# Optimization experiments

Measured on AMD Instinct MI355X. Metric: run time of the kernel, lower is better.

The kernel has to match this reference:

```python
import jax, jax.numpy as jnp
import numpy as np

B, S, HID, H, D = 4, 1024, 1024, 16, 64
MAXP = 1024  # max_position_embeddings
EPS = 1e-8


def setup_inputs() -> dict:
    key = jax.random.key(0)
    ks = jax.random.split(key, 9)
    scale = 0.02  # keep logits small since masked_softmax has no max-subtraction
    return {
        "hidden_states": jax.random.normal(ks[0], (B, S, HID), jnp.float32),
        "attention_mask": jnp.zeros((B, 1, 1, S), jnp.float32),
        "skim_mask": jax.random.randint(ks[1], (B, S), 0, 2, jnp.int32),
        "Wq": jax.random.normal(ks[2], (HID, HID), jnp.float32) * scale,
        "bq": jnp.zeros((HID,), jnp.float32),
        "Wk": jax.random.normal(ks[3], (HID, HID), jnp.float32) * scale,
        "bk": jnp.zeros((HID,), jnp.float32),
        "Wv": jax.random.normal(ks[4], (HID, HID), jnp.float32) * scale,
        "bv": jnp.zeros((HID,), jnp.float32),
        "dist_emb": jax.random.normal(ks[5], (2 * MAXP - 1, D), jnp.float32) * scale,
    }


def reference(hidden_states, attention_mask, skim_mask, Wq, bq, Wk, bk, Wv, bv, dist_emb):
    # Linear projections (W stored as [in, out]) then split heads: [B,H,S,D]
    def heads(x):
        return x.reshape(B, S, H, D).transpose(0, 2, 1, 3)

    q = heads(hidden_states @ Wq + bq)
    k = heads(hidden_states @ Wk + bk)
    v = heads(hidden_states @ Wv + bv)

    # raw scores [B,H,S,S]
    scores = jnp.einsum('bhld,bhrd->bhlr', q, k)

    # relative_key positional bias
    pos = jnp.arange(S)
    distance = pos[:, None] - pos[None, :]                 # [S,S]
    pe = dist_emb[distance + MAXP - 1]                     # [S,S,D]
    scores = scores + jnp.einsum('bhld,lrd->bhlr', q, pe)

    scores = scores / jnp.sqrt(jnp.float32(D))
    scores = scores + attention_mask

    # skim_mask branch: masked_softmax (exp * mask, normalized with eps)
    mask = skim_mask[:, None, None, :].astype(scores.dtype)  # [B,1,1,S]
    exps = jnp.exp(scores) * mask
    probs = exps / (EPS + exps.sum(-1, keepdims=True))
    # dropout in eval mode -> identity

    ctx = jnp.einsum('bhlr,bhrd->bhld', probs, v)
    return ctx.transpose(0, 2, 1, 3).reshape(B, S, HID)
```

## Files before the change

### kernel.cpp

```cpp
#include <hip/hip_runtime.h>
#include <hip/hip_bf16.h>


#define EPSV 1e-8f

typedef short bfrag __attribute__((ext_vector_type(8)));
typedef float cfrag __attribute__((ext_vector_type(16)));
typedef int v2i __attribute__((ext_vector_type(2)));
typedef float v2f __attribute__((ext_vector_type(2)));

__device__ __forceinline__ short f2bf(float f) {
    __hip_bfloat16 h = __float2bfloat16(f);
    return *reinterpret_cast<short*>(&h);
}
__device__ __forceinline__ unsigned int pk2(short a, short b) {
    return (unsigned int)(unsigned short)a | ((unsigned int)(unsigned short)b << 16);
}

__global__ __launch_bounds__(256) void prep(
    const float* __restrict__ hidden, const float* __restrict__ Wq,
    const float* __restrict__ Wk, const float* __restrict__ Wv,
    const float* __restrict__ dist,
    short* __restrict__ Xs, short* __restrict__ Wt, short* __restrict__ Db)
{
    __shared__ short Tl[32 * 72];
    const int bid = blockIdx.x, tid = threadIdx.x;

    if (bid < 2048) {
        const int mt = bid >> 4, kg = bid & 15;
        const int m_l = tid >> 3, k8 = (tid & 7) * 8;
        const float* src = hidden + (size_t)(mt * 32 + m_l) * 1024 + kg * 64 + k8;
        float4 v0 = *(const float4*)src, v1 = *(const float4*)(src + 4);
        short o[8];
        o[0] = f2bf(v0.x); o[1] = f2bf(v0.y); o[2] = f2bf(v0.z); o[3] = f2bf(v0.w);
        o[4] = f2bf(v1.x); o[5] = f2bf(v1.y); o[6] = f2bf(v1.z); o[7] = f2bf(v1.w);
        *(bfrag*)&Tl[m_l * 72 + k8] = *(bfrag*)o;
        __syncthreads();
        const int l31 = tid & 31, q2 = (tid >> 5) & 1, kc = tid >> 6;
        bfrag r = *(const bfrag*)&Tl[l31 * 72 + kc * 16 + q2 * 8];
        *(bfrag*)(Xs + ((size_t)(mt * 64 + kg * 4 + kc) * 64 + q2 * 32 + l31) * 8) = r;
    } else if (bid < 3584) {
        const int t = bid - 2048, z = t >> 9, nt = (t >> 4) & 31, kg = t & 15;
        const float* W = (z == 0) ? Wq : ((z == 1) ? Wk : Wv);
        const int k_l = tid >> 2, n8 = (tid & 3) * 8;
        const float* src = W + (size_t)(kg * 64 + k_l) * 1024 + nt * 32 + n8;
        float4 v0 = *(const float4*)src, v1 = *(const float4*)(src + 4);
        float vv[8] = {v0.x, v0.y, v0.z, v0.w, v1.x, v1.y, v1.z, v1.w};
#pragma unroll
        for (int i = 0; i < 8; i++)
            Tl[(n8 + i) * 72 + k_l] = f2bf(vv[i]);
        __syncthreads();
        const int l31 = tid & 31, q2 = (tid >> 5) & 1, kc = tid >> 6;
        bfrag r = *(const bfrag*)&Tl[l31 * 72 + kc * 16 + q2 * 8];
        *(bfrag*)(Wt + (size_t)z * 1048576
                  + ((size_t)(nt * 64 + kg * 4 + kc) * 64 + q2 * 32 + l31) * 8) = r;
    } else {
        const int idx = (bid - 3584) * 256 + tid;
        if (idx < 16376) {
            const float* src = dist + (size_t)idx * 8;
            float4 v0 = *(const float4*)src, v1 = *(const float4*)(src + 4);
            short o[8];
            o[0] = f2bf(v0.x); o[1] = f2bf(v0.y); o[2] = f2bf(v0.z); o[3] = f2bf(v0.w);
            o[4] = f2bf(v1.x); o[5] = f2bf(v1.y); o[6] = f2bf(v1.z); o[7] = f2bf(v1.w);
            *(bfrag*)(Db + (size_t)idx * 8) = *(bfrag*)o;
        }
    }
}

__global__ __launch_bounds__(256) void qkv_mfma(
    const short* __restrict__ Xs, const short* __restrict__ Wt,
    const float* __restrict__ bq, const float* __restrict__ bk,
    const float* __restrict__ bv,
    short* __restrict__ Qf, short* __restrict__ Kf, short* __restrict__ Vt)
{
    const int z = blockIdx.z;
    const short* W = Wt + (size_t)z * 1048576;
    const float* bias = (z == 0) ? bq : ((z == 1) ? bk : bv);
    const float scale = (z == 0) ? 0.18033688011112042f : 1.0f;

    const int tid = threadIdx.x, lane = tid & 63, wid = tid >> 6;
    const int q2 = lane >> 5, l31 = lane & 31;
    const int wr = wid >> 1, wc = wid & 1;
    const int m0 = blockIdx.x * 128, n0 = blockIdx.y * 128;

    cfrag acc[2][2];
#pragma unroll
    for (int i = 0; i < 2; i++)
#pragma unroll
        for (int j = 0; j < 2; j++)
#pragma unroll
            for (int e = 0; e < 16; e++) acc[i][j][e] = 0.f;

    const short* ap0 = Xs + ((size_t)((m0 >> 5) + wr * 2 + 0) * 64 * 64 + lane) * 8;
    const short* ap1 = Xs + ((size_t)((m0 >> 5) + wr * 2 + 1) * 64 * 64 + lane) * 8;
    const short* bp0 = W  + ((size_t)((n0 >> 5) + wc * 2 + 0) * 64 * 64 + lane) * 8;
    const short* bp1 = W  + ((size_t)((n0 >> 5) + wc * 2 + 1) * 64 * 64 + lane) * 8;

    bfrag a0c, a1c, b0c, b1c, a0n, a1n, b0n, b1n;
    a0c = *(const bfrag*)(ap0); a1c = *(const bfrag*)(ap1);
    b0c = *(const bfrag*)(bp0); b1c = *(const bfrag*)(bp1);

#pragma unroll 2
    for (int kc = 0; kc < 64; kc += 2) {
        {
            const int off = (kc + 1) * 512;
            a0n = *(const bfrag*)(ap0 + off); a1n = *(const bfrag*)(ap1 + off);
            b0n = *(const bfrag*)(bp0 + off); b1n = *(const bfrag*)(bp1 + off);
        }
        acc[0][0] = __builtin_amdgcn_mfma_f32_32x32x16_bf16(a0c, b0c, acc[0][0], 0, 0, 0);
        acc[0][1] = __builtin_amdgcn_mfma_f32_32x32x16_bf16(a0c, b1c, acc[0][1], 0, 0, 0);
        acc[1][0] = __builtin_amdgcn_mfma_f32_32x32x16_bf16(a1c, b0c, acc[1][0], 0, 0, 0);
        acc[1][1] = __builtin_amdgcn_mfma_f32_32x32x16_bf16(a1c, b1c, acc[1][1], 0, 0, 0);
        if (kc + 2 < 64) {
            const int off = (kc + 2) * 512;
            a0c = *(const bfrag*)(ap0 + off); a1c = *(const bfrag*)(ap1 + off);
            b0c = *(const bfrag*)(bp0 + off); b1c = *(const bfrag*)(bp1 + off);
        }
        acc[0][0] = __builtin_amdgcn_mfma_f32_32x32x16_bf16(a0n, b0n, acc[0][0], 0, 0, 0);
        acc[0][1] = __builtin_amdgcn_mfma_f32_32x32x16_bf16(a0n, b1n, acc[0][1], 0, 0, 0);
        acc[1][0] = __builtin_amdgcn_mfma_f32_32x32x16_bf16(a1n, b0n, acc[1][0], 0, 0, 0);
        acc[1][1] = __builtin_amdgcn_mfma_f32_32x32x16_bf16(a1n, b1n, acc[1][1], 0, 0, 0);
    }

#pragma unroll
    for (int nt = 0; nt < 2; nt++) {
        const int c = n0 + wc * 64 + nt * 32 + l31;
        const float bval = bias[c];
        const int h = c >> 6;
        const int d = nt * 32 + l31;
#pragma unroll
        for (int mt = 0; mt < 2; mt++) {
            const int tok0 = m0 + wr * 64 + mt * 32;
            const int bb = tok0 >> 10, s_base = tok0 & 1023;
            const size_t bhbase = (size_t)(bb * 16 + h) * 65536;
            if (z < 2) {
                short* outp = (z == 0) ? Qf : Kf;
                const size_t fbase = bhbase
                    + ((size_t)((s_base >> 5) * 4 + (d >> 4)) * 64
                       + ((d >> 3) & 1) * 32) * 8 + (d & 7);
#pragma unroll
                for (int reg = 0; reg < 16; reg++) {
                    const int row = (reg & 3) + 8 * (reg >> 2) + 4 * q2;
                    outp[fbase + (size_t)row * 8] = f2bf((acc[mt][nt][reg] + bval) * scale);
                }
            } else {
#pragma unroll
                for (int g = 0; g < 4; g++) {
                    const float e0 = acc[mt][nt][4 * g + 0] + bval;
                    const float e1 = acc[mt][nt][4 * g + 1] + bval;
                    const float e2 = acc[mt][nt][4 * g + 2] + bval;
                    const float e3 = acc[mt][nt][4 * g + 3] + bval;
                    uint2 w2;
                    w2.x = pk2(f2bf(e0), f2bf(e1));
                    w2.y = pk2(f2bf(e2), f2bf(e3));
                    const size_t flat = bhbase
                        + ((size_t)(nt * 64 + (s_base >> 4) + (g >> 1)) * 64
                           + (g & 1) * 32 + l31) * 8 + 4 * q2;
                    *(uint2*)(Vt + flat) = w2;
                }
            }
        }
    }
}

__global__ __launch_bounds__(256, 2) void attn_mfma(
    const short* __restrict__ Qf, const short* __restrict__ Kf,
    const short* __restrict__ Vt, const short* __restrict__ Db,
    const float* __restrict__ amask, const int* __restrict__ skim,
    float* __restrict__ out)
{
    __shared__ short Tb[128 * 132];
    __shared__ float Lg[1024];

    const int tid = threadIdx.x, lane = tid & 63, w = tid >> 6;
    const int q2 = lane >> 5, l31 = lane & 31;
    const int bh = blockIdx.x, b = bh >> 4, hh = bh & 15;
    const int l0 = blockIdx.y * 128;

    {
        const int r4 = tid * 4;
        float4 am = *(const float4*)(amask + b * 1024 + r4);
        int4 sk = *(const int4*)(skim + b * 1024 + r4);
        Lg[r4 + 0] = __expf(am.x) * (float)sk.x;
        Lg[r4 + 1] = __expf(am.y) * (float)sk.y;
        Lg[r4 + 2] = __expf(am.z) * (float)sk.z;
        Lg[r4 + 3] = __expf(am.w) * (float)sk.w;
    }
    __syncthreads();

    const short* Qg = Qf + (size_t)bh * 65536;
    const short* Kg = Kf + (size_t)bh * 65536;
    const short* Vg = Vt + (size_t)bh * 65536;

    bfrag qa[4];
#pragma unroll
    for (int c = 0; c < 4; c++)
        qa[c] = *(const bfrag*)(Qg + ((size_t)(((l0 >> 5) + w) * 4 + c) * 64 + lane) * 8);

    cfrag oacc[2];
#pragma unroll
    for (int mt = 0; mt < 2; mt++)
#pragma unroll
        for (int e = 0; e < 16; e++) oacc[mt][e] = 0.f;
    v2f es01 = {0.f, 0.f}, es23 = {0.f, 0.f};

    const int Lband = l0 + 32 * w;
    const int lg = Lband + l31;
    const int rowb = (32 * w + l31) * 132;

    for (int r0 = -128; r0 < 1024; r0 += 64) {
        const bool produce = r0 < 960;

        bfrag pb[2][4];
        if (produce) {
#pragma unroll
            for (int mt = 0; mt < 2; mt++) {
                const int D0 = Lband - r0 - 128 + 32 * mt;
                const int er = min(max(D0 + l31 + 1023, 0), 2046);
#pragma unroll
                for (int kc = 0; kc < 4; kc++)
                    pb[mt][kc] = *(const bfrag*)(Db + (size_t)er * 64 + kc * 16 + q2 * 8);
            }
        }

        if (r0 >= 0) {
            bfrag kb[2][4], vbl[4][2];
            v2i trr[2][4];
#pragma unroll
            for (int mt = 0; mt < 2; mt++)
#pragma unroll
                for (int kc = 0; kc < 4; kc++)
                    kb[mt][kc] = *(const bfrag*)(Kg
                        + ((size_t)(((r0 >> 5) + mt) * 4 + kc) * 64 + lane) * 8);
#pragma unroll
            for (int kc = 0; kc < 4; kc++)
#pragma unroll
                for (int mtd = 0; mtd < 2; mtd++)
                    vbl[kc][mtd] = *(const bfrag*)(Vg
                        + ((size_t)(mtd * 64 + (r0 >> 4) + kc) * 64 + lane) * 8);
#pragma unroll
            for (int mt = 0; mt < 2; mt++)
#pragma unroll
                for (int g = 0; g < 4; g++)
                    trr[mt][g] = *(const v2i*)&Tb[rowb
                        + ((r0 + 32 * mt + 8 * g + 4 * q2) & 127)];

#pragma unroll
            for (int mt = 0; mt < 2; mt++) {
                cfrag sfr;
#pragma unroll
                for (int g = 0; g < 4; g++) {
                    const v2i t2 = trr[mt][g];
                    sfr[4 * g + 0] = __builtin_bit_cast(float, (unsigned)t2[0] << 16);
                    sfr[4 * g + 1] = __builtin_bit_cast(float, (unsigned)t2[0] & 0xffff0000u);
                    sfr[4 * g + 2] = __builtin_bit_cast(float, (unsigned)t2[1] << 16);
                    sfr[4 * g + 3] = __builtin_bit_cast(float, (unsigned)t2[1] & 0xffff0000u);
                }
                __builtin_amdgcn_s_setprio(1);
#pragma unroll
                for (int kc = 0; kc < 4; kc++)
                    sfr = __builtin_amdgcn_mfma_f32_32x32x16_bf16(
                        kb[mt][kc], qa[kc], sfr, 0, 0, 0);
                __builtin_amdgcn_s_setprio(0);

                unsigned int P[4][2];
#pragma unroll
                for (int g = 0; g < 4; g++) {
                    const int rb = r0 + 32 * mt + 8 * g + 4 * q2;
                    float4 g4 = *(const float4*)&Lg[rb];
                    float ev0 = __builtin_amdgcn_exp2f(sfr[4 * g + 0]) * g4.x;
                    float ev1 = __builtin_amdgcn_exp2f(sfr[4 * g + 1]) * g4.y;
                    float ev2 = __builtin_amdgcn_exp2f(sfr[4 * g + 2]) * g4.z;
                    float ev3 = __builtin_amdgcn_exp2f(sfr[4 * g + 3]) * g4.w;
                    es01 += (v2f){ev0, ev1};
                    es23 += (v2f){ev2, ev3};
                    P[g][0] = pk2(f2bf(ev0), f2bf(ev1));
                    P[g][1] = pk2(f2bf(ev2), f2bf(ev3));
                }
#pragma unroll
                for (int c = 0; c < 2; c++) {
                    v2i s0 = __builtin_amdgcn_permlane32_swap(
                        (int)P[2 * c][0], (int)P[2 * c + 1][0], false, false);
                    v2i s1 = __builtin_amdgcn_permlane32_swap(
                        (int)P[2 * c][1], (int)P[2 * c + 1][1], false, false);
                    union { bfrag f; int d[4]; } u;
                    u.d[0] = s0[0]; u.d[1] = s1[0]; u.d[2] = s0[1]; u.d[3] = s1[1];
                    const int kc = 2 * mt + c;
                    __builtin_amdgcn_s_setprio(1);
#pragma unroll
                    for (int mtd = 0; mtd < 2; mtd++)
                        oacc[mtd] = __builtin_amdgcn_mfma_f32_32x32x16_bf16(
                            vbl[kc][mtd], u.f, oacc[mtd], 0, 0, 0);
                    __builtin_amdgcn_s_setprio(0);
                }
            }
        }

        if (produce) {
#pragma unroll
            for (int mt = 0; mt < 2; mt++) {
                cfrag t;
#pragma unroll
                for (int e = 0; e < 16; e++) t[e] = 0.f;
                __builtin_amdgcn_s_setprio(1);
#pragma unroll
                for (int kc = 0; kc < 4; kc++)
                    t = __builtin_amdgcn_mfma_f32_32x32x16_bf16(
                        pb[mt][kc], qa[kc], t, 0, 0, 0);
                __builtin_amdgcn_s_setprio(0);
#pragma unroll
                for (int e = 0; e < 16; e++) {
                    const int rr = (e & 3) + 8 * (e >> 2) + 4 * q2;
                    Tb[rowb + ((l31 + r0 - 32 * mt - rr) & 127)] = f2bf(t[e]);
                }
            }
        }
    }

    float esum = (es01[0] + es01[1]) + (es23[0] + es23[1]);
    const float den = EPSV + esum + __shfl_xor(esum, 32);
    const float inv = 1.0f / den;
    float* ob = out + ((size_t)(b * 1024 + lg) * 1024) + hh * 64;
#pragma unroll
    for (int mtd = 0; mtd < 2; mtd++) {
#pragma unroll
        for (int g = 0; g < 4; g++) {
            float4 o;
            o.x = oacc[mtd][4 * g + 0] * inv;
            o.y = oacc[mtd][4 * g + 1] * inv;
            o.z = oacc[mtd][4 * g + 2] * inv;
            o.w = oacc[mtd][4 * g + 3] * inv;
            *(float4*)(ob + 32 * mtd + 8 * g + 4 * q2) = o;
        }
    }
}

extern "C" void kernel_launch(void* const* d_in, const int* in_sizes, int n_in,
                              void* d_out, int out_size, void* d_ws, size_t ws_size,
                              hipStream_t stream) {
    const float* hidden = (const float*)d_in[0];
    const float* amask  = (const float*)d_in[1];
    const int*   skim   = (const int*)d_in[2];
    const float* Wq     = (const float*)d_in[3];
    const float* bq     = (const float*)d_in[4];
    const float* Wk     = (const float*)d_in[5];
    const float* bk     = (const float*)d_in[6];
    const float* Wv     = (const float*)d_in[7];
    const float* bv     = (const float*)d_in[8];
    const float* dist   = (const float*)d_in[9];
    float* out = (float*)d_out;

    char* w = (char*)d_ws;
    short* Xs  = (short*)(w);
    short* Wt  = (short*)(w + ((size_t)8 << 20));
    short* Db  = (short*)(w + ((size_t)14 << 20));
    short* Qf  = (short*)(w + ((size_t)15 << 20));
    short* Kf  = (short*)(w + ((size_t)23 << 20));
    short* Vt  = (short*)(w + ((size_t)31 << 20));

    prep<<<3648, 256, 0, stream>>>(hidden, Wq, Wk, Wv, dist, Xs, Wt, Db);
    qkv_mfma<<<dim3(32, 8, 3), 256, 0, stream>>>(Xs, Wt, bq, bk, bv, Qf, Kf, Vt);
    attn_mfma<<<dim3(64, 8), 256, 0, stream>>>(Qf, Kf, Vt, Db, amask, skim, out);
}
```

Baseline: 187.1 us.

## Deepen GEMM prefetch ring and software-pipeline K loads in attention loop

The projection GEMM now keeps a 4-deep ring of register fragments, prefetching four k-steps ahead instead of double-buffering two. The attention kernel splits its prologue (the two position-bias tiles before r0=0) out of the main loop, then runs the loop in pairs with ping-pong K fragment buffers, loading the next block's K while computing the current one. V loads move into the per-mt step so fewer registers are live at once. The launch bound changes to an amdgpu_waves_per_eu(2) hint. These aim to hide global-load latency behind MFMA work, at the cost of more register pressure and possible spills.

```diff
diff --git a/kernel.cpp b/kernel.cpp
--- a/kernel.cpp
+++ b/kernel.cpp
@@ -96,30 +96,26 @@
     const short* bp0 = W  + ((size_t)((n0 >> 5) + wc * 2 + 0) * 64 * 64 + lane) * 8;
     const short* bp1 = W  + ((size_t)((n0 >> 5) + wc * 2 + 1) * 64 * 64 + lane) * 8;
 
-    bfrag a0c, a1c, b0c, b1c, a0n, a1n, b0n, b1n;
-    a0c = *(const bfrag*)(ap0); a1c = *(const bfrag*)(ap1);
-    b0c = *(const bfrag*)(bp0); b1c = *(const bfrag*)(bp1);
-
-#pragma unroll 2
-    for (int kc = 0; kc < 64; kc += 2) {
-        {
-            const int off = (kc + 1) * 512;
-            a0n = *(const bfrag*)(ap0 + off); a1n = *(const bfrag*)(ap1 + off);
-            b0n = *(const bfrag*)(bp0 + off); b1n = *(const bfrag*)(bp1 + off);
-        }
-        acc[0][0] = __builtin_amdgcn_mfma_f32_32x32x16_bf16(a0c, b0c, acc[0][0], 0, 0, 0);
-        acc[0][1] = __builtin_amdgcn_mfma_f32_32x32x16_bf16(a0c, b1c, acc[0][1], 0, 0, 0);
-        acc[1][0] = __builtin_amdgcn_mfma_f32_32x32x16_bf16(a1c, b0c, acc[1][0], 0, 0, 0);
-        acc[1][1] = __builtin_amdgcn_mfma_f32_32x32x16_bf16(a1c, b1c, acc[1][1], 0, 0, 0);
-        if (kc + 2 < 64) {
-            const int off = (kc + 2) * 512;
-            a0c = *(const bfrag*)(ap0 + off); a1c = *(const bfrag*)(ap1 + off);
-            b0c = *(const bfrag*)(bp0 + off); b1c = *(const bfrag*)(bp1 + off);
-        }
-        acc[0][0] = __builtin_amdgcn_mfma_f32_32x32x16_bf16(a0n, b0n, acc[0][0], 0, 0, 0);
-        acc[0][1] = __builtin_amdgcn_mfma_f32_32x32x16_bf16(a0n, b1n, acc[0][1], 0, 0, 0);
-        acc[1][0] = __builtin_amdgcn_mfma_f32_32x32x16_bf16(a1n, b0n, acc[1][0], 0, 0, 0);
-        acc[1][1] = __builtin_amdgcn_mfma_f32_32x32x16_bf16(a1n, b1n, acc[1][1], 0, 0, 0);
+    bfrag A0[4], A1[4], B0[4], B1[4];
+#pragma unroll
+    for (int g = 0; g < 4; g++) {
+        const int off = g * 512;
+        A0[g] = *(const bfrag*)(ap0 + off); A1[g] = *(const bfrag*)(ap1 + off);
+        B0[g] = *(const bfrag*)(bp0 + off); B1[g] = *(const bfrag*)(bp1 + off);
+    }
+
+#pragma unroll 4
+    for (int kc = 0; kc < 64; kc++) {
+        const int s = kc & 3;
+        acc[0][0] = __builtin_amdgcn_mfma_f32_32x32x16_bf16(A0[s], B0[s], acc[0][0], 0, 0, 0);
+        acc[0][1] = __builtin_amdgcn_mfma_f32_32x32x16_bf16(A0[s], B1[s], acc[0][1], 0, 0, 0);
+        acc[1][0] = __builtin_amdgcn_mfma_f32_32x32x16_bf16(A1[s], B0[s], acc[1][0], 0, 0, 0);
+        acc[1][1] = __builtin_amdgcn_mfma_f32_32x32x16_bf16(A1[s], B1[s], acc[1][1], 0, 0, 0);
+        if (kc + 4 < 64) {
+            const int off = (kc + 4) * 512;
+            A0[s] = *(const bfrag*)(ap0 + off); A1[s] = *(const bfrag*)(ap1 + off);
+            B0[s] = *(const bfrag*)(bp0 + off); B1[s] = *(const bfrag*)(bp1 + off);
+        }
     }
 
 #pragma unroll
@@ -163,7 +159,8 @@
     }
 }
 
-__global__ __launch_bounds__(256, 2) void attn_mfma(
+__global__ __launch_bounds__(256) __attribute__((amdgpu_waves_per_eu(2)))
+void attn_mfma(
     const short* __restrict__ Qf, const short* __restrict__ Kf,
     const short* __restrict__ Vt, const short* __restrict__ Db,
     const float* __restrict__ amask, const int* __restrict__ skim,
@@ -208,113 +205,129 @@
     const int lg = Lband + l31;
     const int rowb = (32 * w + l31) * 132;
 
-    for (int r0 = -128; r0 < 1024; r0 += 64) {
-        const bool produce = r0 < 960;
-
+    auto LOADPB = [&](int r0k, bfrag (&PB)[2][4]) {
+#pragma unroll
+        for (int mt = 0; mt < 2; mt++) {
+            const int er = min(max(Lband - r0k - 128 + 32 * mt + l31 + 1023, 0), 2046);
+#pragma unroll
+            for (int kc = 0; kc < 4; kc++)
+                PB[mt][kc] = *(const bfrag*)(Db + (size_t)er * 64 + kc * 16 + q2 * 8);
+        }
+    };
+    auto PRODUCE = [&](int r0k, bfrag (&PB)[2][4]) {
+#pragma unroll
+        for (int mt = 0; mt < 2; mt++) {
+            cfrag t;
+#pragma unroll
+            for (int e = 0; e < 16; e++) t[e] = 0.f;
+            __builtin_amdgcn_s_setprio(1);
+#pragma unroll
+            for (int kc = 0; kc < 4; kc++)
+                t = __builtin_amdgcn_mfma_f32_32x32x16_bf16(PB[mt][kc], qa[kc], t, 0, 0, 0);
+            __builtin_amdgcn_s_setprio(0);
+#pragma unroll
+            for (int e = 0; e < 16; e++) {
+                const int rr = (e & 3) + 8 * (e >> 2) + 4 * q2;
+                Tb[rowb + ((l31 + r0k - 32 * mt - rr) & 127)] = f2bf(t[e]);
+            }
+        }
+    };
+    auto LOADKB = [&](int rk, bfrag (&KB)[2][4]) {
+#pragma unroll
+        for (int mt = 0; mt < 2; mt++)
+#pragma unroll
+            for (int kc = 0; kc < 4; kc++)
+                KB[mt][kc] = *(const bfrag*)(Kg
+                    + ((size_t)(((rk >> 5) + mt) * 4 + kc) * 64 + lane) * 8);
+    };
+
+    bfrag kbA[2][4], kbB[2][4];
+
+    auto BODY = [&](int r, bfrag (&CUR)[2][4], bfrag (&NXT)[2][4]) {
+        const bool prod = r < 960;
         bfrag pb[2][4];
-        if (produce) {
-#pragma unroll
-            for (int mt = 0; mt < 2; mt++) {
-                const int D0 = Lband - r0 - 128 + 32 * mt;
-                const int er = min(max(D0 + l31 + 1023, 0), 2046);
-#pragma unroll
-                for (int kc = 0; kc < 4; kc++)
-                    pb[mt][kc] = *(const bfrag*)(Db + (size_t)er * 64 + kc * 16 + q2 * 8);
-            }
-        }
-
-        if (r0 >= 0) {
-            bfrag kb[2][4], vbl[4][2];
-            v2i trr[2][4];
-#pragma unroll
-            for (int mt = 0; mt < 2; mt++)
-#pragma unroll
-                for (int kc = 0; kc < 4; kc++)
-                    kb[mt][kc] = *(const bfrag*)(Kg
-                        + ((size_t)(((r0 >> 5) + mt) * 4 + kc) * 64 + lane) * 8);
+        if (prod) LOADPB(r, pb);
+        if (r + 64 < 1024) LOADKB(r + 64, NXT);
+        v2i trr[2][4];
+#pragma unroll
+        for (int mt = 0; mt < 2; mt++)
+#pragma unroll
+            for (int g = 0; g < 4; g++)
+                trr[mt][g] = *(const v2i*)&Tb[rowb
+                    + ((r + 32 * mt + 8 * g + 4 * q2) & 127)];
+
+#pragma unroll
+        for (int mt = 0; mt < 2; mt++) {
+            bfrag vbl[2][2];
+#pragma unroll
+            for (int c = 0; c < 2; c++)
+#pragma unroll
+                for (int mtd = 0; mtd < 2; mtd++)
+                    vbl[c][mtd] = *(const bfrag*)(Vg
+                        + ((size_t)(mtd * 64 + (r >> 4) + 2 * mt + c) * 64 + lane) * 8);
+
+            cfrag sfr;
+#pragma unroll
+            for (int g = 0; g < 4; g++) {
+                const v2i t2 = trr[mt][g];
+                sfr[4 * g + 0] = __builtin_bit_cast(float, (unsigned)t2[0] << 16);
+                sfr[4 * g + 1] = __builtin_bit_cast(float, (unsigned)t2[0] & 0xffff0000u);
+                sfr[4 * g + 2] = __builtin_bit_cast(float, (unsigned)t2[1] << 16);
+                sfr[4 * g + 3] = __builtin_bit_cast(float, (unsigned)t2[1] & 0xffff0000u);
+            }
+            __builtin_amdgcn_s_setprio(1);
 #pragma unroll
             for (int kc = 0; kc < 4; kc++)
+                sfr = __builtin_amdgcn_mfma_f32_32x32x16_bf16(
+                    CUR[mt][kc], qa[kc], sfr, 0, 0, 0);
+            __builtin_amdgcn_s_setprio(0);
+
+            unsigned int P[4][2];
+#pragma unroll
+            for (int g = 0; g < 4; g++) {
+                const int rb = r + 32 * mt + 8 * g + 4 * q2;
+                float4 g4 = *(const float4*)&Lg[rb];
+                float ev0 = __builtin_amdgcn_exp2f(sfr[4 * g + 0]) * g4.x;
+                float ev1 = __builtin_amdgcn_exp2f(sfr[4 * g + 1]) * g4.y;
+                float ev2 = __builtin_amdgcn_exp2f(sfr[4 * g + 2]) * g4.z;
+                float ev3 = __builtin_amdgcn_exp2f(sfr[4 * g + 3]) * g4.w;
+                es01 += (v2f){ev0, ev1};
+                es23 += (v2f){ev2, ev3};
+                P[g][0] = pk2(f2bf(ev0), f2bf(ev1));
+                P[g][1] = pk2(f2bf(ev2), f2bf(ev3));
+            }
+#pragma unroll
+            for (int c = 0; c < 2; c++) {
+                v2i s0 = __builtin_amdgcn_permlane32_swap(
+                    (int)P[2 * c][0], (int)P[2 * c + 1][0], false, false);
+                v2i s1 = __builtin_amdgcn_permlane32_swap(
+                    (int)P[2 * c][1], (int)P[2 * c + 1][1], false, false);
+                union { bfrag f; int d[4]; } u;
+                u.d[0] = s0[0]; u.d[1] = s1[0]; u.d[2] = s0[1]; u.d[3] = s1[1];
+                __builtin_amdgcn_s_setprio(1);
 #pragma unroll
                 for (int mtd = 0; mtd < 2; mtd++)
-                    vbl[kc][mtd] = *(const bfrag*)(Vg
-                        + ((size_t)(mtd * 64 + (r0 >> 4) + kc) * 64 + lane) * 8);
-#pragma unroll
-            for (int mt = 0; mt < 2; mt++)
-#pragma unroll
-                for (int g = 0; g < 4; g++)
-                    trr[mt][g] = *(const v2i*)&Tb[rowb
-                        + ((r0 + 32 * mt + 8 * g + 4 * q2) & 127)];
-
-#pragma unroll
-            for (int mt = 0; mt < 2; mt++) {
-                cfrag sfr;
-#pragma unroll
-                for (int g = 0; g < 4; g++) {
-                    const v2i t2 = trr[mt][g];
-                    sfr[4 * g + 0] = __builtin_bit_cast(float, (unsigned)t2[0] << 16);
-                    sfr[4 * g + 1] = __builtin_bit_cast(float, (unsigned)t2[0] & 0xffff0000u);
-                    sfr[4 * g + 2] = __builtin_bit_cast(float, (unsigned)t2[1] << 16);
-                    sfr[4 * g + 3] = __builtin_bit_cast(float, (unsigned)t2[1] & 0xffff0000u);
-                }
-                __builtin_amdgcn_s_setprio(1);
-#pragma unroll
-                for (int kc = 0; kc < 4; kc++)
-                    sfr = __builtin_amdgcn_mfma_f32_32x32x16_bf16(
-                        kb[mt][kc], qa[kc], sfr, 0, 0, 0);
+                    oacc[mtd] = __builtin_amdgcn_mfma_f32_32x32x16_bf16(
+                        vbl[c][mtd], u.f, oacc[mtd], 0, 0, 0);
                 __builtin_amdgcn_s_setprio(0);
-
-                unsigned int P[4][2];
-#pragma unroll
-                for (int g = 0; g < 4; g++) {
-                    const int rb = r0 + 32 * mt + 8 * g + 4 * q2;
-                    float4 g4 = *(const float4*)&Lg[rb];
-                    float ev0 = __builtin_amdgcn_exp2f(sfr[4 * g + 0]) * g4.x;
-                    float ev1 = __builtin_amdgcn_exp2f(sfr[4 * g + 1]) * g4.y;
-                    float ev2 = __builtin_amdgcn_exp2f(sfr[4 * g + 2]) * g4.z;
-                    float ev3 = __builtin_amdgcn_exp2f(sfr[4 * g + 3]) * g4.w;
-                    es01 += (v2f){ev0, ev1};
-                    es23 += (v2f){ev2, ev3};
-                    P[g][0] = pk2(f2bf(ev0), f2bf(ev1));
-                    P[g][1] = pk2(f2bf(ev2), f2bf(ev3));
-                }
-#pragma unroll
-                for (int c = 0; c < 2; c++) {
-                    v2i s0 = __builtin_amdgcn_permlane32_swap(
-                        (int)P[2 * c][0], (int)P[2 * c + 1][0], false, false);
-                    v2i s1 = __builtin_amdgcn_permlane32_swap(
-                        (int)P[2 * c][1], (int)P[2 * c + 1][1], false, false);
-                    union { bfrag f; int d[4]; } u;
-                    u.d[0] = s0[0]; u.d[1] = s1[0]; u.d[2] = s0[1]; u.d[3] = s1[1];
-                    const int kc = 2 * mt + c;
-                    __builtin_amdgcn_s_setprio(1);
-#pragma unroll
-                    for (int mtd = 0; mtd < 2; mtd++)
-                        oacc[mtd] = __builtin_amdgcn_mfma_f32_32x32x16_bf16(
-                            vbl[kc][mtd], u.f, oacc[mtd], 0, 0, 0);
-                    __builtin_amdgcn_s_setprio(0);
-                }
-            }
-        }
-
-        if (produce) {
-#pragma unroll
-            for (int mt = 0; mt < 2; mt++) {
-                cfrag t;
-#pragma unroll
-                for (int e = 0; e < 16; e++) t[e] = 0.f;
-                __builtin_amdgcn_s_setprio(1);
-#pragma unroll
-                for (int kc = 0; kc < 4; kc++)
-                    t = __builtin_amdgcn_mfma_f32_32x32x16_bf16(
-                        pb[mt][kc], qa[kc], t, 0, 0, 0);
-                __builtin_amdgcn_s_setprio(0);
-#pragma unroll
-                for (int e = 0; e < 16; e++) {
-                    const int rr = (e & 3) + 8 * (e >> 2) + 4 * q2;
-                    Tb[rowb + ((l31 + r0 - 32 * mt - rr) & 127)] = f2bf(t[e]);
-                }
-            }
-        }
+            }
+        }
+
+        if (prod) PRODUCE(r, pb);
+    };
+
+    {
+        bfrag pb[2][4];
+        LOADPB(-128, pb);
+        LOADKB(0, kbA);
+        PRODUCE(-128, pb);
+        LOADPB(-64, pb);
+        PRODUCE(-64, pb);
+    }
+
+    for (int r0 = 0; r0 < 1024; r0 += 128) {
+        BODY(r0, kbA, kbB);
+        BODY(r0 + 64, kbB, kbA);
     }
 
     float esum = (es01[0] + es01[1]) + (es23[0] + es23[1]);
```

Measured after the change: 186.2 us. Within noise of the previous version (-0.5%).
